# Kernel optimization log

Measured on AMD Instinct MI355X. Metric: run time of the kernel, lower is better.

The kernel has to match this reference:

```python
import jax, jax.numpy as jnp
import numpy as np

TIME_LEN = 8
JOINT_NUM = 22
SEQ = TIME_LEN * JOINT_NUM  # 176
H_NUM = 8
H_DIM = 32
NEG_BIG = -9e15


def _temporal_mask():
    # ones everywhere, except block-diagonal joint x joint blocks zeroed, plus identity
    m = np.ones((SEQ, SEQ), dtype=np.float32)
    for i in range(TIME_LEN):
        m[i * JOINT_NUM:(i + 1) * JOINT_NUM, i * JOINT_NUM:(i + 1) * JOINT_NUM] = 0.0
    spatial = 1.0 - m
    temporal = m + np.eye(SEQ, dtype=np.float32)
    return jnp.asarray(temporal), jnp.asarray(spatial)


def setup_inputs() -> dict:
    key = jax.random.key(0)
    ks = jax.random.split(key, 4)
    B, S, D_in = 256, SEQ, 128
    D_model = H_NUM * H_DIM
    s = 1.0 / np.sqrt(D_in)
    return {
        "x": jax.random.normal(ks[0], (B, S, D_in), dtype=jnp.float32),
        "Wq": jax.random.normal(ks[1], (D_in, D_model), dtype=jnp.float32) * s,
        "bq": jnp.zeros((D_model,), dtype=jnp.float32),
        "Wk": jax.random.normal(ks[2], (D_in, D_model), dtype=jnp.float32) * s,
        "bk": jnp.zeros((D_model,), dtype=jnp.float32),
        "Wv": jax.random.normal(ks[3], (D_in, D_model), dtype=jnp.float32) * s,
        "bv": jnp.zeros((D_model,), dtype=jnp.float32),
    }


def reference(x, Wq, bq, Wk, bk, Wv, bv):
    B = x.shape[0]
    mask, _ = _temporal_mask()  # att_type == 'temporal'

    def split_heads(t):  # [B,S,H*D] -> [B,H,S,D]
        return t.reshape(B, SEQ, H_NUM, H_DIM).transpose(0, 2, 1, 3)

    q = split_heads(x @ Wq + bq)
    k = split_heads(x @ Wk + bk)
    v = split_heads(jax.nn.relu(x @ Wv + bv))  # value map has ReLU

    scores = jnp.einsum("bhsd,bhtd->bhst", q, k) / jnp.sqrt(jnp.float32(H_DIM))
    scores = scores * mask + (1.0 - mask) * NEG_BIG
    att = jax.nn.softmax(scores, axis=-1)
    out = jnp.einsum("bhst,bhtd->bhsd", att, v)
    return out.transpose(0, 2, 1, 3).reshape(B, SEQ, H_NUM * H_DIM)
```

## Files before the change

### kernel.cpp

```cpp
#include <hip/hip_runtime.h>


#define SEQ    176
#define HD     32
#define DIN    128
#define DMODEL 256

#define KSTRIDE 44
#define VSTRIDE 204
#define QSCALE  0.25506100344358246f

typedef unsigned short ushort_t;
typedef unsigned int uint_t;
typedef __attribute__((ext_vector_type(8))) short short8;
typedef __attribute__((ext_vector_type(4))) short short4v;
typedef __attribute__((ext_vector_type(4))) float float4v;
typedef __attribute__((ext_vector_type(4))) unsigned short ushort4v;
typedef __attribute__((ext_vector_type(2))) unsigned int uint2v;
typedef __attribute__((ext_vector_type(4))) unsigned int uint4v;

#define WS_WT 0u
#define WS_X  196608u

#define OFF_KS 13056
#define OFF_VT (OFF_KS + 176 * KSTRIDE)
#define SMEM_TOTAL (OFF_VT + 32 * VSTRIDE)

__device__ __forceinline__ ushort_t f2bf(float f) {
    union { float f; unsigned int u; } cv; cv.f = f;
    unsigned int u = cv.u;
    unsigned int rb = 0x7FFFu + ((u >> 16) & 1u);
    return (ushort_t)((u + rb) >> 16);
}
__device__ __forceinline__ uint_t pk2(float a, float b) {
    return (uint_t)f2bf(a) | ((uint_t)f2bf(b) << 16);
}

__global__ __launch_bounds__(256)
void k0_conv(const float* __restrict__ x,
             const float* __restrict__ Wq, const float* __restrict__ Wk,
             const float* __restrict__ Wv,
             ushort_t* __restrict__ WT, ushort_t* __restrict__ X16)
{
    int bid = blockIdx.x;
    if (bid < 5632) {
        int f4 = bid * 256 + threadIdx.x;
        float4 v = reinterpret_cast<const float4*>(x)[f4];
        ushort4v o;
        o.x = f2bf(v.x); o.y = f2bf(v.y); o.z = f2bf(v.z); o.w = f2bf(v.w);
        reinterpret_cast<ushort4v*>(X16)[f4] = o;
    } else {
        int idx = (bid - 5632) * 256 + threadIdx.x;
        int e = idx * 4;
        int mat = e >> 15, h = (e >> 12) & 7, n = (e >> 7) & 31, k = e & 127;
        const float* W = (mat == 0) ? Wq : ((mat == 1) ? Wk : Wv);
        const float sc = (mat == 0) ? QSCALE : 1.0f;
        ushort4v o;
        o.x = f2bf(W[(k + 0) * DMODEL + h * HD + n] * sc);
        o.y = f2bf(W[(k + 1) * DMODEL + h * HD + n] * sc);
        o.z = f2bf(W[(k + 2) * DMODEL + h * HD + n] * sc);
        o.w = f2bf(W[(k + 3) * DMODEL + h * HD + n] * sc);
        reinterpret_cast<ushort4v*>(WT)[idx] = o;
    }
}

__global__ __launch_bounds__(704, 6)
void k1_attn(const ushort_t* __restrict__ X16, const ushort_t* __restrict__ WT,
             const float* __restrict__ bq, const float* __restrict__ bk,
             const float* __restrict__ bv, float* __restrict__ out)
{
    __shared__ __align__(16) ushort_t smem[SMEM_TOTAL];
    ushort_t* WS = smem;
    ushort_t* KS = smem + OFF_KS;
    ushort_t* VT = smem + OFF_VT;

    const int tid  = threadIdx.x;
    const int lane = tid & 63;
    const int w    = tid >> 6;
    const int c    = lane & 15;
    const int q    = lane >> 4;

    const int xcd = blockIdx.x & 7;
    const int j   = blockIdx.x >> 3;
    const int b   = xcd * 32 + (j >> 3);
    const int h   = j & 7;

    const ushort_t* xr = X16 + ((size_t)b * SEQ + w * 16 + c) * DIN;
    short8 xf[4];
#pragma unroll
    for (int kk = 0; kk < 4; ++kk)
        xf[kk] = *reinterpret_cast<const short8*>(xr + kk * 32 + q * 8);

    float4 bqv0 = *reinterpret_cast<const float4*>(bq + h * HD + q * 4);
    float4 bqv1 = *reinterpret_cast<const float4*>(bq + h * HD + 16 + q * 4);
    bqv0.x *= QSCALE; bqv0.y *= QSCALE; bqv0.z *= QSCALE; bqv0.w *= QSCALE;
    bqv1.x *= QSCALE; bqv1.y *= QSCALE; bqv1.z *= QSCALE; bqv1.w *= QSCALE;
    float4 bkv0 = *reinterpret_cast<const float4*>(bk + h * HD + q * 4);
    float4 bkv1 = *reinterpret_cast<const float4*>(bk + h * HD + 16 + q * 4);
    const float bvc0 = bv[h * HD + c];
    const float bvc1 = bv[h * HD + 16 + c];

#pragma unroll
    for (int it = 0; it < 3; ++it) {
        int c8 = tid + it * 704;
        if (c8 < 1536) {
            int mat = c8 >> 9, rem = c8 & 511, n = rem >> 4, kc = rem & 15;
            short8 v = *reinterpret_cast<const short8*>(
                WT + (size_t)(((mat * 8 + h) * 32 + n) * 128 + kc * 8));
            *reinterpret_cast<short8*>(WS + (mat * 32 + n) * 136 + kc * 8) = v;
        }
    }
    if (tid < 512) {
        VT[(tid >> 4) * VSTRIDE + 176 + (tid & 15)] = 0;
    }
    __syncthreads();

    uint_t qd[4];
#pragma unroll
    for (int nt = 0; nt < 2; ++nt) {
        const ushort_t* wrow = WS + (nt * 16 + c) * 136 + q * 8;
        float4v acc = {0.f, 0.f, 0.f, 0.f};
#pragma unroll
        for (int kk = 0; kk < 4; ++kk) {
            short8 wf = *reinterpret_cast<const short8*>(wrow + kk * 32);
            acc = __builtin_amdgcn_mfma_f32_16x16x32_bf16(wf, xf[kk], acc, 0, 0, 0);
        }
        const float4 bb = nt ? bqv1 : bqv0;
        qd[nt * 2 + 0] = pk2(acc[0] + bb.x, acc[1] + bb.y);
        qd[nt * 2 + 1] = pk2(acc[2] + bb.z, acc[3] + bb.w);
    }
    short8 qf8;
    { union { uint4v u; short8 s; } t;
      t.u = (uint4v){qd[0], qd[1], qd[2], qd[3]}; qf8 = t.s; }

#pragma unroll
    for (int nt = 0; nt < 2; ++nt) {
        const ushort_t* wrow = WS + (32 + nt * 16 + c) * 136 + q * 8;
        float4v acc = {0.f, 0.f, 0.f, 0.f};
#pragma unroll
        for (int kk = 0; kk < 4; ++kk) {
            short8 wf = *reinterpret_cast<const short8*>(wrow + kk * 32);
            acc = __builtin_amdgcn_mfma_f32_16x16x32_bf16(wf, xf[kk], acc, 0, 0, 0);
        }
        const float4 bb = nt ? bkv1 : bkv0;
        uint2v kd;
        kd.x = pk2(acc[0] + bb.x, acc[1] + bb.y);
        kd.y = pk2(acc[2] + bb.z, acc[3] + bb.w);
        *reinterpret_cast<uint2v*>(&KS[(w * 16 + c) * KSTRIDE + nt * 16 + q * 4]) = kd;
    }
#pragma unroll
    for (int nt = 0; nt < 2; ++nt) {
        const ushort_t* wrow = WS + (64 + nt * 16 + c) * 136 + q * 8;
        float4v acc = {0.f, 0.f, 0.f, 0.f};
#pragma unroll
        for (int kk = 0; kk < 4; ++kk) {
            short8 wf = *reinterpret_cast<const short8*>(wrow + kk * 32);
            acc = __builtin_amdgcn_mfma_f32_16x16x32_bf16(xf[kk], wf, acc, 0, 0, 0);
        }
        const float bb = nt ? bvc1 : bvc0;
        float v0 = acc[0] + bb; v0 = v0 > 0.f ? v0 : 0.f;
        float v1 = acc[1] + bb; v1 = v1 > 0.f ? v1 : 0.f;
        float v2 = acc[2] + bb; v2 = v2 > 0.f ? v2 : 0.f;
        float v3 = acc[3] + bb; v3 = v3 > 0.f ? v3 : 0.f;
        uint2v vd;
        vd.x = pk2(v0, v1);
        vd.y = pk2(v2, v3);
        *reinterpret_cast<uint2v*>(&VT[(nt * 16 + c) * VSTRIDE + w * 16 + q * 4]) = vd;
    }
    __syncthreads();

    const int t_row = w * 16 + c;
    const int lo = (t_row / 22) * 22;
    float su = 0.f;
    uint_t pw[24];
    pw[22] = 0u; pw[23] = 0u;
#pragma unroll
    for (int n = 0; n < 11; ++n) {
        const ushort_t* krow = KS + (n * 16 + c) * KSTRIDE;
        short4v ka = *reinterpret_cast<const short4v*>(krow + q * 4);
        short4v kb = *reinterpret_cast<const short4v*>(krow + 16 + q * 4);
        short8 kf = {ka.x, ka.y, ka.z, ka.w, kb.x, kb.y, kb.z, kb.w};
        float4v s = {0.f, 0.f, 0.f, 0.f};
        s = __builtin_amdgcn_mfma_f32_16x16x32_bf16(kf, qf8, s, 0, 0, 0);
        float e[4];
#pragma unroll
        for (int r = 0; r < 4; ++r) {
            int tp = n * 16 + q * 4 + r;
            float sv = (((unsigned)(tp - lo) < 22u) && (tp != t_row)) ? -1e30f : s[r];
            e[r] = __builtin_amdgcn_exp2f(sv);
            su += e[r];
        }
        pw[n * 2 + 0] = pk2(e[0], e[1]);
        pw[n * 2 + 1] = pk2(e[2], e[3]);
    }
    su += __shfl_xor(su, 16, 64);
    su += __shfl_xor(su, 32, 64);
    const float invs = 1.0f / su;

    float* ob = out + ((size_t)b * SEQ + t_row) * DMODEL + h * HD;
#pragma unroll
    for (int mt = 0; mt < 2; ++mt) {
        const ushort_t* vrow = VT + (mt * 16 + c) * VSTRIDE;
        float4v o = {0.f, 0.f, 0.f, 0.f};
#pragma unroll
        for (int g = 0; g < 6; ++g) {
            short4v va = *reinterpret_cast<const short4v*>(vrow + (2 * g) * 16 + q * 4);
            short4v vb2 = *reinterpret_cast<const short4v*>(vrow + (2 * g + 1) * 16 + q * 4);
            short8 vf = {va.x, va.y, va.z, va.w, vb2.x, vb2.y, vb2.z, vb2.w};
            union { uint4v u; short8 s; } pt;
            pt.u = (uint4v){pw[4 * g], pw[4 * g + 1], pw[4 * g + 2], pw[4 * g + 3]};
            o = __builtin_amdgcn_mfma_f32_16x16x32_bf16(vf, pt.s, o, 0, 0, 0);
        }
        float4 st;
        st.x = o[0] * invs; st.y = o[1] * invs;
        st.z = o[2] * invs; st.w = o[3] * invs;
        *reinterpret_cast<float4*>(ob + mt * 16 + q * 4) = st;
    }
}

extern "C" void kernel_launch(void* const* d_in, const int* in_sizes, int n_in,
                              void* d_out, int out_size, void* d_ws, size_t ws_size,
                              hipStream_t stream) {
    const float* x  = (const float*)d_in[0];
    const float* Wq = (const float*)d_in[1];
    const float* bq = (const float*)d_in[2];
    const float* Wk = (const float*)d_in[3];
    const float* bk = (const float*)d_in[4];
    const float* Wv = (const float*)d_in[5];
    const float* bv = (const float*)d_in[6];
    float* out = (float*)d_out;

    char* ws = (char*)d_ws;
    ushort_t* WT  = (ushort_t*)(ws + WS_WT);
    ushort_t* X16 = (ushort_t*)(ws + WS_X);

    k0_conv<<<dim3(5728), dim3(256), 0, stream>>>(x, Wq, Wk, Wv, WT, X16);
    k1_attn<<<dim3(2048), dim3(704), 0, stream>>>(X16, WT, bq, bk, bv, out);
}
```

Before: 134.3 us.

## Fuse x bf16 conversion into attention kernel and read weights from global

Drops the separate fp32-to-bf16 pass over x and has the attention kernel load fp32 x directly, packing it with the hardware v_cvt_pk_bf16_f32 instruction. Weight tiles are no longer staged in LDS, so one __syncthreads goes away and LDS use shrinks, which may raise occupancy. MFMA weight fragments now come straight from global/L2 memory. Each block reads fp32 x at twice the bytes, but this saves the extra write and read of the bf16 copy.

```diff
diff --git a/kernel.cpp b/kernel.cpp
--- a/kernel.cpp
+++ b/kernel.cpp
@@ -15,63 +15,46 @@
 typedef __attribute__((ext_vector_type(8))) short short8;
 typedef __attribute__((ext_vector_type(4))) short short4v;
 typedef __attribute__((ext_vector_type(4))) float float4v;
-typedef __attribute__((ext_vector_type(4))) unsigned short ushort4v;
 typedef __attribute__((ext_vector_type(2))) unsigned int uint2v;
 typedef __attribute__((ext_vector_type(4))) unsigned int uint4v;
 
 #define WS_WT 0u
-#define WS_X  196608u
-
-#define OFF_KS 13056
-#define OFF_VT (OFF_KS + 176 * KSTRIDE)
+
+#define OFF_VT (176 * KSTRIDE)
 #define SMEM_TOTAL (OFF_VT + 32 * VSTRIDE)
 
-__device__ __forceinline__ ushort_t f2bf(float f) {
-    union { float f; unsigned int u; } cv; cv.f = f;
-    unsigned int u = cv.u;
-    unsigned int rb = 0x7FFFu + ((u >> 16) & 1u);
-    return (ushort_t)((u + rb) >> 16);
-}
 __device__ __forceinline__ uint_t pk2(float a, float b) {
-    return (uint_t)f2bf(a) | ((uint_t)f2bf(b) << 16);
+    uint_t r;
+    asm("v_cvt_pk_bf16_f32 %0, %1, %2" : "=v"(r) : "v"(a), "v"(b));
+    return r;
 }
 
 __global__ __launch_bounds__(256)
-void k0_conv(const float* __restrict__ x,
-             const float* __restrict__ Wq, const float* __restrict__ Wk,
-             const float* __restrict__ Wv,
-             ushort_t* __restrict__ WT, ushort_t* __restrict__ X16)
+void k0_conv(const float* __restrict__ Wq, const float* __restrict__ Wk,
+             const float* __restrict__ Wv, ushort_t* __restrict__ WT)
 {
-    int bid = blockIdx.x;
-    if (bid < 5632) {
-        int f4 = bid * 256 + threadIdx.x;
-        float4 v = reinterpret_cast<const float4*>(x)[f4];
-        ushort4v o;
-        o.x = f2bf(v.x); o.y = f2bf(v.y); o.z = f2bf(v.z); o.w = f2bf(v.w);
-        reinterpret_cast<ushort4v*>(X16)[f4] = o;
-    } else {
-        int idx = (bid - 5632) * 256 + threadIdx.x;
-        int e = idx * 4;
-        int mat = e >> 15, h = (e >> 12) & 7, n = (e >> 7) & 31, k = e & 127;
-        const float* W = (mat == 0) ? Wq : ((mat == 1) ? Wk : Wv);
-        const float sc = (mat == 0) ? QSCALE : 1.0f;
-        ushort4v o;
-        o.x = f2bf(W[(k + 0) * DMODEL + h * HD + n] * sc);
-        o.y = f2bf(W[(k + 1) * DMODEL + h * HD + n] * sc);
-        o.z = f2bf(W[(k + 2) * DMODEL + h * HD + n] * sc);
-        o.w = f2bf(W[(k + 3) * DMODEL + h * HD + n] * sc);
-        reinterpret_cast<ushort4v*>(WT)[idx] = o;
-    }
+    int idx = blockIdx.x * 256 + threadIdx.x;
+    int e = idx * 4;
+    int mat = e >> 15, h = (e >> 12) & 7, n = (e >> 7) & 31, k = e & 127;
+    const float* W = (mat == 0) ? Wq : ((mat == 1) ? Wk : Wv);
+    const float sc = (mat == 0) ? QSCALE : 1.0f;
+    float w0 = W[(k + 0) * DMODEL + h * HD + n] * sc;
+    float w1 = W[(k + 1) * DMODEL + h * HD + n] * sc;
+    float w2 = W[(k + 2) * DMODEL + h * HD + n] * sc;
+    float w3 = W[(k + 3) * DMODEL + h * HD + n] * sc;
+    uint2v o;
+    o.x = pk2(w0, w1);
+    o.y = pk2(w2, w3);
+    reinterpret_cast<uint2v*>(WT)[idx] = o;
 }
 
 __global__ __launch_bounds__(704, 6)
-void k1_attn(const ushort_t* __restrict__ X16, const ushort_t* __restrict__ WT,
+void k1_attn(const float* __restrict__ x, const ushort_t* __restrict__ WT,
              const float* __restrict__ bq, const float* __restrict__ bk,
              const float* __restrict__ bv, float* __restrict__ out)
 {
     __shared__ __align__(16) ushort_t smem[SMEM_TOTAL];
-    ushort_t* WS = smem;
-    ushort_t* KS = smem + OFF_KS;
+    ushort_t* KS = smem;
     ushort_t* VT = smem + OFF_VT;
 
     const int tid  = threadIdx.x;
@@ -85,11 +68,17 @@
     const int b   = xcd * 32 + (j >> 3);
     const int h   = j & 7;
 
-    const ushort_t* xr = X16 + ((size_t)b * SEQ + w * 16 + c) * DIN;
+    const float* xrow = x + ((size_t)b * SEQ + w * 16 + c) * DIN + q * 8;
     short8 xf[4];
 #pragma unroll
-    for (int kk = 0; kk < 4; ++kk)
-        xf[kk] = *reinterpret_cast<const short8*>(xr + kk * 32 + q * 8);
+    for (int kk = 0; kk < 4; ++kk) {
+        float4 a0 = *reinterpret_cast<const float4*>(xrow + kk * 32);
+        float4 a1 = *reinterpret_cast<const float4*>(xrow + kk * 32 + 4);
+        union { uint4v u; short8 s; } t;
+        t.u = (uint4v){pk2(a0.x, a0.y), pk2(a0.z, a0.w),
+                       pk2(a1.x, a1.y), pk2(a1.z, a1.w)};
+        xf[kk] = t.s;
+    }
 
     float4 bqv0 = *reinterpret_cast<const float4*>(bq + h * HD + q * 4);
     float4 bqv1 = *reinterpret_cast<const float4*>(bq + h * HD + 16 + q * 4);
@@ -100,25 +89,14 @@
     const float bvc0 = bv[h * HD + c];
     const float bvc1 = bv[h * HD + 16 + c];
 
-#pragma unroll
-    for (int it = 0; it < 3; ++it) {
-        int c8 = tid + it * 704;
-        if (c8 < 1536) {
-            int mat = c8 >> 9, rem = c8 & 511, n = rem >> 4, kc = rem & 15;
-            short8 v = *reinterpret_cast<const short8*>(
-                WT + (size_t)(((mat * 8 + h) * 32 + n) * 128 + kc * 8));
-            *reinterpret_cast<short8*>(WS + (mat * 32 + n) * 136 + kc * 8) = v;
-        }
-    }
     if (tid < 512) {
         VT[(tid >> 4) * VSTRIDE + 176 + (tid & 15)] = 0;
     }
-    __syncthreads();
 
     uint_t qd[4];
 #pragma unroll
     for (int nt = 0; nt < 2; ++nt) {
-        const ushort_t* wrow = WS + (nt * 16 + c) * 136 + q * 8;
+        const ushort_t* wrow = WT + (size_t)((0 * 8 + h) * 32 + nt * 16 + c) * 128 + q * 8;
         float4v acc = {0.f, 0.f, 0.f, 0.f};
 #pragma unroll
         for (int kk = 0; kk < 4; ++kk) {
@@ -135,7 +113,7 @@
 
 #pragma unroll
     for (int nt = 0; nt < 2; ++nt) {
-        const ushort_t* wrow = WS + (32 + nt * 16 + c) * 136 + q * 8;
+        const ushort_t* wrow = WT + (size_t)((1 * 8 + h) * 32 + nt * 16 + c) * 128 + q * 8;
         float4v acc = {0.f, 0.f, 0.f, 0.f};
 #pragma unroll
         for (int kk = 0; kk < 4; ++kk) {
@@ -150,7 +128,7 @@
     }
 #pragma unroll
     for (int nt = 0; nt < 2; ++nt) {
-        const ushort_t* wrow = WS + (64 + nt * 16 + c) * 136 + q * 8;
+        const ushort_t* wrow = WT + (size_t)((2 * 8 + h) * 32 + nt * 16 + c) * 128 + q * 8;
         float4v acc = {0.f, 0.f, 0.f, 0.f};
 #pragma unroll
         for (int kk = 0; kk < 4; ++kk) {
@@ -231,9 +209,8 @@
     float* out = (float*)d_out;
 
     char* ws = (char*)d_ws;
-    ushort_t* WT  = (ushort_t*)(ws + WS_WT);
-    ushort_t* X16 = (ushort_t*)(ws + WS_X);
-
-    k0_conv<<<dim3(5728), dim3(256), 0, stream>>>(x, Wq, Wk, Wv, WT, X16);
-    k1_attn<<<dim3(2048), dim3(704), 0, stream>>>(X16, WT, bq, bk, bv, out);
-}
+    ushort_t* WT = (ushort_t*)(ws + WS_WT);
+
+    k0_conv<<<dim3(96), dim3(256), 0, stream>>>(Wq, Wk, Wv, WT);
+    k1_attn<<<dim3(2048), dim3(704), 0, stream>>>(x, WT, bq, bk, bv, out);
+}
```

Result: slower. 191.2 us (+42.4%).
